# Performance work log

Measured on AMD Instinct MI355X. Metric: run time of the kernel, lower is better.

The kernel has to match this reference:

```python
import jax, jax.numpy as jnp
import numpy as np

N_NODES = 50000
N_EDGES = 800000
N_HIDDEN = 64
N_LAYER = 3
IN_DIM = 4


def setup_inputs() -> dict:
    key = jax.random.key(0)
    ks = jax.random.split(key, 10)
    x = jax.random.normal(ks[0], (N_NODES, IN_DIM), dtype=jnp.float32)
    edge_index = jax.random.randint(ks[1], (2, N_EDGES), 0, N_NODES, dtype=jnp.int64)
    # Glorot-style params matching pyg GCNConv (lin has no bias; conv adds bias after aggregation)
    def glorot(k, fan_in, fan_out):
        s = jnp.sqrt(6.0 / (fan_in + fan_out))
        return jax.random.uniform(k, (fan_in, fan_out), jnp.float32, -s, s)
    W_in = glorot(ks[2], IN_DIM, N_HIDDEN)
    b_in = jnp.zeros((N_HIDDEN,), jnp.float32)
    W_h = jnp.stack([glorot(jax.random.fold_in(ks[3], i), N_HIDDEN, N_HIDDEN) for i in range(N_LAYER)])
    b_h = jnp.zeros((N_LAYER, N_HIDDEN), jnp.float32)
    W_out = glorot(ks[4], N_HIDDEN, 1)
    b_out = jnp.zeros((1,), jnp.float32)
    return {"x": x, "edge_index": edge_index, "W_in": W_in, "b_in": b_in,
            "W_h": W_h, "b_h": b_h, "W_out": W_out, "b_out": b_out}


def _gcn_norm(edge_index, n_nodes):
    # add self-loops, compute symmetric norm D^{-1/2} (A+I) D^{-1/2}
    loop = jnp.arange(n_nodes, dtype=edge_index.dtype)
    src = jnp.concatenate([edge_index[0], loop])
    dst = jnp.concatenate([edge_index[1], loop])
    deg = jax.ops.segment_sum(jnp.ones_like(dst, dtype=jnp.float32), dst, num_segments=n_nodes)
    dinv = jax.lax.rsqrt(deg)  # deg >= 1 due to self-loops
    norm = dinv[src] * dinv[dst]
    return src, dst, norm


def _gcn_conv(x, W, b, src, dst, norm, n_nodes):
    h = x @ W                                   # [N, out]
    msg = h[src] * norm[:, None]                # gather + scale, [E+N, out]
    out = jax.ops.segment_sum(msg, dst, num_segments=n_nodes)  # scatter-add
    return out + b


def reference(x, edge_index, W_in, b_in, W_h, b_h, W_out, b_out):
    n = x.shape[0]
    src, dst, norm = _gcn_norm(edge_index, n)
    h = jax.nn.relu(_gcn_conv(x, W_in, b_in, src, dst, norm, n))
    for i in range(W_h.shape[0]):
        h = jax.nn.relu(_gcn_conv(h, W_h[i], b_h[i], src, dst, norm, n))
    return _gcn_conv(h, W_out, b_out, src, dst, norm, n)
```

## Files before the change

kernel.cpp:

```cpp
#include <hip/hip_runtime.h>
#include <hip/hip_bf16.h>


#define TPB 256
#define EPT 8
#define CHUNK (TPB * EPT)
typedef __hip_bfloat16 bf16;
#define B2F __bfloat162float

__global__ void k_zero_cnt(int* __restrict__ cnt, int n) {
    int i = blockIdx.x * blockDim.x + threadIdx.x;
    if (i < n) cnt[i] = 0;
}

__global__ void k_hist(const int* __restrict__ dst, int* __restrict__ cnt, int E, int n) {
    int e = blockIdx.x * blockDim.x + threadIdx.x;
    if (e < E) {
        int d = dst[e];
        if ((unsigned)d < (unsigned)n) atomicAdd(&cnt[d], 1);
    }
}

__global__ void k_blocksum(const int* __restrict__ cnt, int* __restrict__ bsum, int n) {
    __shared__ int s[TPB];
    int i = blockIdx.x * TPB + threadIdx.x;
    s[threadIdx.x] = (i < n) ? cnt[i] : 0;
    __syncthreads();
    for (int off = TPB / 2; off > 0; off >>= 1) {
        if (threadIdx.x < off) s[threadIdx.x] += s[threadIdx.x + off];
        __syncthreads();
    }
    if (threadIdx.x == 0) bsum[blockIdx.x] = s[0];
}

__global__ void k_scan_bsum(int* __restrict__ bsum, int nb) {
    __shared__ int s[TPB];
    int t = threadIdx.x;
    int v = (t < nb) ? bsum[t] : 0;
    s[t] = v;
    __syncthreads();
    for (int off = 1; off < TPB; off <<= 1) {
        int u = (t >= off) ? s[t - off] : 0;
        __syncthreads();
        s[t] += u;
        __syncthreads();
    }
    if (t < nb) bsum[t] = s[t] - v;
}

__global__ void k_scan_final(const int* __restrict__ cnt, const int* __restrict__ bsum,
                             int* __restrict__ row_start, int* __restrict__ cursor,
                             float* __restrict__ dinv, int n) {
    __shared__ int s[TPB];
    int t = threadIdx.x;
    int i = blockIdx.x * TPB + t;
    int v = (i < n) ? cnt[i] : 0;
    s[t] = v;
    __syncthreads();
    for (int off = 1; off < TPB; off <<= 1) {
        int u = (t >= off) ? s[t - off] : 0;
        __syncthreads();
        s[t] += u;
        __syncthreads();
    }
    if (i < n) {
        int excl = bsum[blockIdx.x] + s[t] - v;
        row_start[i] = excl;
        cursor[i] = excl;
        dinv[i] = rsqrtf((float)v + 1.0f);
        if (i == n - 1) row_start[n] = excl + v;
    }
}

__global__ void k_init_bcur(const int* __restrict__ row_start, int* __restrict__ bcur,
                            int B, int n) {
    int b = threadIdx.x;
    if (b < B) bcur[b] = row_start[min(b << 8, n)];
}

__global__ __launch_bounds__(TPB) void k_bin(
    const int* __restrict__ src, const int* __restrict__ dst,
    int* __restrict__ bcur, unsigned* __restrict__ staging, int E, int n) {
    __shared__ int hcnt[256];
    __shared__ int hbase[256];
    int tid = threadIdx.x;
    int e0 = blockIdx.x * CHUNK;
    hcnt[tid] = 0;
    __syncthreads();

    int eb[EPT];
    unsigned rec[EPT];
#pragma unroll
    for (int u = 0; u < EPT; ++u) {
        int e = e0 + u * TPB + tid;
        eb[u] = -1;
        if (e < E) {
            int d = dst[e], s = src[e];
            if ((unsigned)d < (unsigned)n && (unsigned)s < (unsigned)n) {
                eb[u] = d >> 8;
                rec[u] = (unsigned)s | ((unsigned)(d & 255) << 16);
                atomicAdd(&hcnt[eb[u]], 1);
            }
        }
    }
    __syncthreads();
    int c = hcnt[tid];
    hbase[tid] = (c > 0) ? atomicAdd(&bcur[tid], c) : 0;
    hcnt[tid] = 0;
    __syncthreads();
#pragma unroll
    for (int u = 0; u < EPT; ++u) {
        if (eb[u] >= 0) {
            int r = atomicAdd(&hcnt[eb[u]], 1);
            int pos = hbase[eb[u]] + r;
            if ((unsigned)pos < (unsigned)E) staging[pos] = rec[u];
        }
    }
}

__global__ __launch_bounds__(TPB) void k_unbin(
    const unsigned* __restrict__ staging, const int* __restrict__ row_start,
    int* __restrict__ cursor, unsigned short* __restrict__ bucket, int E, int n) {
    int b = blockIdx.x;
    int lo = row_start[min(b << 8, n)];
    int hi = row_start[min((b + 1) << 8, n)];
    lo = max(0, min(lo, E)); hi = max(lo, min(hi, E));
    for (int i = lo + threadIdx.x; i < hi; i += TPB) {
        unsigned r = staging[i];
        int d = min((b << 8) + (int)(r >> 16), n - 1);
        int pos = atomicAdd(&cursor[d], 1);
        if ((unsigned)pos < (unsigned)E) bucket[pos] = (unsigned short)(r & 0xffffu);
    }
}

__global__ void k_mm_in(const float* __restrict__ x, const float* __restrict__ W,
                        const float* __restrict__ dinv, bf16* __restrict__ g, int n) {
    int t = blockIdx.x * blockDim.x + threadIdx.x;
    if (t >= n * 64) return;
    int i = t >> 6, j = t & 63;
    float acc = 0.f;
#pragma unroll
    for (int k = 0; k < 4; ++k) acc = fmaf(x[i * 4 + k], W[k * 64 + j], acc);
    g[t] = __float2bfloat16(acc * dinv[i]);
}

__device__ __forceinline__ void acc_quad(float4& a, uint2 w) {
    a.x += __uint_as_float(w.x << 16);
    a.y += __uint_as_float(w.x & 0xffff0000u);
    a.z += __uint_as_float(w.y << 16);
    a.w += __uint_as_float(w.y & 0xffff0000u);
}

__device__ __forceinline__ void agg_row_quad(const bf16* __restrict__ g,
                                             const unsigned short* __restrict__ bucket,
                                             int k0, int k1, int d, float* __restrict__ sVp,
                                             int lane, unsigned nm1, unsigned Em1) {
    int grp = lane >> 4, i = lane & 15;
    float4 a = {0.f, 0.f, 0.f, 0.f};
    if (grp == 0) {
        uint2 w = *(const uint2*)(g + (size_t)d * 64 + 4 * i);
        acc_quad(a, w);
    }
    for (int base = k0; base < k1; base += 64) {
        int cnt = min(64, k1 - base);
        int rec = bucket[min((unsigned)(base + lane), Em1)];
        int k = 0;
        for (; k + 16 <= cnt; k += 16) {
            unsigned s0 = min((unsigned)__shfl(rec, k + 0 + grp), nm1);
            unsigned s1 = min((unsigned)__shfl(rec, k + 4 + grp), nm1);
            unsigned s2 = min((unsigned)__shfl(rec, k + 8 + grp), nm1);
            unsigned s3 = min((unsigned)__shfl(rec, k + 12 + grp), nm1);
            uint2 w0 = *(const uint2*)(g + (size_t)s0 * 64 + 4 * i);
            uint2 w1 = *(const uint2*)(g + (size_t)s1 * 64 + 4 * i);
            uint2 w2 = *(const uint2*)(g + (size_t)s2 * 64 + 4 * i);
            uint2 w3 = *(const uint2*)(g + (size_t)s3 * 64 + 4 * i);
            acc_quad(a, w0); acc_quad(a, w1); acc_quad(a, w2); acc_quad(a, w3);
        }
        for (; k < cnt; k += 4) {
            int e = k + grp;
            unsigned s = min((unsigned)__shfl(rec, min(e, 63)), nm1);
            uint2 w = *(const uint2*)(g + (size_t)s * 64 + 4 * i);
            if (e < cnt) acc_quad(a, w);
        }
    }
    ((float4*)(sVp + grp * 64))[i] = a;
}

__global__ __launch_bounds__(TPB) void k_gconv(
    const bf16* __restrict__ gIn, const float* __restrict__ dinv,
    const int* __restrict__ row_start, const unsigned short* __restrict__ bucket,
    const float* __restrict__ bias, const float* __restrict__ W,
    bf16* __restrict__ gOut, int n, int E) {
    __shared__ float sVp[4][4 * 64];
    int tid = threadIdx.x;
    int r = tid >> 6, j = tid & 63;
    int d = blockIdx.x * 4 + r;
    if (d >= n) return;
    float dd = dinv[d];
    int k0 = row_start[d], k1 = row_start[d + 1];
    k1 = min(k1, E); k0 = max(min(k0, k1), 0);
    agg_row_quad(gIn, bucket, k0, k1, d, sVp[r], j, (unsigned)(n - 1), (unsigned)(E - 1));
    float v = sVp[r][j] + sVp[r][64 + j] + sVp[r][128 + j] + sVp[r][192 + j];
    float a = fmaxf(fmaf(dd, v, bias[j]), 0.f);
    sVp[r][j] = a;
    const float4* ap = (const float4*)&sVp[r][0];
    float acc0 = 0.f, acc1 = 0.f, acc2 = 0.f, acc3 = 0.f;
#pragma unroll
    for (int k4 = 0; k4 < 16; ++k4) {
        float4 a4 = ap[k4];
        acc0 = fmaf(a4.x, W[(4 * k4 + 0) * 64 + j], acc0);
        acc1 = fmaf(a4.y, W[(4 * k4 + 1) * 64 + j], acc1);
        acc2 = fmaf(a4.z, W[(4 * k4 + 2) * 64 + j], acc2);
        acc3 = fmaf(a4.w, W[(4 * k4 + 3) * 64 + j], acc3);
    }
    float acc = (acc0 + acc1) + (acc2 + acc3);
    gOut[(size_t)d * 64 + j] = __float2bfloat16(acc * dd);
}

__global__ __launch_bounds__(TPB) void k_gconv_z(
    const bf16* __restrict__ gIn, const float* __restrict__ dinv,
    const int* __restrict__ row_start, const unsigned short* __restrict__ bucket,
    const float* __restrict__ bias, const float* __restrict__ Wout,
    float* __restrict__ zg, int n, int E) {
    __shared__ float sVp[4][4 * 64];
    int tid = threadIdx.x;
    int r = tid >> 6, j = tid & 63;
    int d = blockIdx.x * 4 + r;
    if (d >= n) return;
    float dd = dinv[d];
    int k0 = row_start[d], k1 = row_start[d + 1];
    k1 = min(k1, E); k0 = max(min(k0, k1), 0);
    agg_row_quad(gIn, bucket, k0, k1, d, sVp[r], j, (unsigned)(n - 1), (unsigned)(E - 1));
    float v = sVp[r][j] + sVp[r][64 + j] + sVp[r][128 + j] + sVp[r][192 + j];
    float a = fmaxf(fmaf(dd, v, bias[j]), 0.f) * Wout[j];
#pragma unroll
    for (int off = 32; off > 0; off >>= 1) a += __shfl_down(a, off);
    if (j == 0) zg[d] = a * dd;
}

__global__ __launch_bounds__(TPB) void k_out(
    const float* __restrict__ zg, const float* __restrict__ dinv,
    const int* __restrict__ row_start, const unsigned short* __restrict__ bucket,
    const float* __restrict__ b_out, float* __restrict__ out, int n, int E) {
    int t = blockIdx.x * blockDim.x + threadIdx.x;
    int d = t >> 6, lane = t & 63;
    if (d >= n) return;
    int k0 = row_start[d], k1 = row_start[d + 1];
    k1 = min(k1, E); k0 = max(min(k0, k1), 0);
    unsigned nm1 = (unsigned)(n - 1);
    float v = 0.f;
    for (int k = k0 + lane; k < k1; k += 64) {
        unsigned s = min((unsigned)bucket[k], nm1);
        v += zg[s];
    }
#pragma unroll
    for (int off = 32; off > 0; off >>= 1) v += __shfl_down(v, off);
    if (lane == 0) out[d] = fmaf(zg[d] + v, dinv[d], b_out[0]);
}

extern "C" void kernel_launch(void* const* d_in, const int* in_sizes, int n_in,
                              void* d_out, int out_size, void* d_ws, size_t ws_size,
                              hipStream_t stream) {
    const float* x     = (const float*)d_in[0];
    const int*   ei    = (const int*)d_in[1];
    const float* W_in  = (const float*)d_in[2];
    const float* b_in  = (const float*)d_in[3];
    const float* W_h   = (const float*)d_in[4];
    const float* b_h   = (const float*)d_in[5];
    const float* W_out = (const float*)d_in[6];
    const float* b_out = (const float*)d_in[7];
    float* out = (float*)d_out;

    int N = in_sizes[0] / 4;
    int E = in_sizes[1] / 2;
    const int* src = ei;
    const int* dst = ei + E;

    char* ws = (char*)d_ws;
    bf16* gA               = (bf16*)ws;           ws += (size_t)N * 64 * 2;
    bf16* gB               = (bf16*)ws;           ws += (size_t)N * 64 * 2;
    unsigned short* bucket = (unsigned short*)ws; ws += (size_t)E * 2;
    unsigned* staging      = (unsigned*)ws;       ws += (size_t)E * 4;
    int*  row_start        = (int*)ws;            ws += (size_t)(N + 1) * 4;
    int*  cursor           = (int*)ws;            ws += (size_t)N * 4;
    int*  cnt              = (int*)ws;            ws += (size_t)N * 4;
    float* dinv            = (float*)ws;          ws += (size_t)N * 4;
    float* zg              = (float*)ws;          ws += (size_t)N * 4;
    int*  bsum             = (int*)ws;            ws += 257 * 4;
    int*  bcur             = (int*)ws;

    int B   = (N + 255) >> 8;
    int gN  = (N + TPB - 1) / TPB;
    int gE  = (E + TPB - 1) / TPB;
    int gNF = (N * 64 + TPB - 1) / TPB;
    int gN4 = (N + 3) / 4;
    int gBin = (E + CHUNK - 1) / CHUNK;

    k_zero_cnt<<<gN, TPB, 0, stream>>>(cnt, N);
    k_hist<<<gE, TPB, 0, stream>>>(dst, cnt, E, N);
    k_blocksum<<<gN, TPB, 0, stream>>>(cnt, bsum, N);
    k_scan_bsum<<<1, TPB, 0, stream>>>(bsum, gN);
    k_scan_final<<<gN, TPB, 0, stream>>>(cnt, bsum, row_start, cursor, dinv, N);
    k_init_bcur<<<1, TPB, 0, stream>>>(row_start, bcur, B, N);
    k_bin<<<gBin, TPB, 0, stream>>>(src, dst, bcur, staging, E, N);
    k_unbin<<<B, TPB, 0, stream>>>(staging, row_start, cursor, bucket, E, N);

    k_mm_in<<<gNF, TPB, 0, stream>>>(x, W_in, dinv, gA, N);
    k_gconv<<<gN4, TPB, 0, stream>>>(gA, dinv, row_start, bucket, b_in, W_h, gB, N, E);
    k_gconv<<<gN4, TPB, 0, stream>>>(gB, dinv, row_start, bucket, b_h, W_h + 4096, gA, N, E);
    k_gconv<<<gN4, TPB, 0, stream>>>(gA, dinv, row_start, bucket, b_h + 64, W_h + 8192, gB, N, E);
    k_gconv_z<<<gN4, TPB, 0, stream>>>(gB, dinv, row_start, bucket, b_h + 128, W_out, zg, N, E);
    k_out<<<gN4, TPB, 0, stream>>>(zg, dinv, row_start, bucket, b_out, out, N, E);
}
```

Measured before the change: 310.4 us.

## Replace per-node histogram and global scan with bucket-level counting and in-block CSR build

Drops the per-node global histogram, the three-pass prefix scan and the bcur init. It now counts edges per 256-node bucket using shared-memory atomics and scans only 256 bucket totals. Each unbin block builds its own per-node counts, row offsets and dinv in shared memory, and places edges with shared-memory cursors instead of global atomics. This cuts kernel launches and global atomic traffic during graph preprocessing, but the staging array is now read twice in unbin and the approach only supports up to 256 buckets.

```diff
diff --git a/kernel.cpp b/kernel.cpp
--- a/kernel.cpp
+++ b/kernel.cpp
@@ -8,74 +8,46 @@
 typedef __hip_bfloat16 bf16;
 #define B2F __bfloat162float
 
-__global__ void k_zero_cnt(int* __restrict__ cnt, int n) {
-    int i = blockIdx.x * blockDim.x + threadIdx.x;
-    if (i < n) cnt[i] = 0;
-}
-
-__global__ void k_hist(const int* __restrict__ dst, int* __restrict__ cnt, int E, int n) {
-    int e = blockIdx.x * blockDim.x + threadIdx.x;
-    if (e < E) {
-        int d = dst[e];
-        if ((unsigned)d < (unsigned)n) atomicAdd(&cnt[d], 1);
-    }
-}
-
-__global__ void k_blocksum(const int* __restrict__ cnt, int* __restrict__ bsum, int n) {
-    __shared__ int s[TPB];
-    int i = blockIdx.x * TPB + threadIdx.x;
-    s[threadIdx.x] = (i < n) ? cnt[i] : 0;
-    __syncthreads();
-    for (int off = TPB / 2; off > 0; off >>= 1) {
-        if (threadIdx.x < off) s[threadIdx.x] += s[threadIdx.x + off];
-        __syncthreads();
-    }
-    if (threadIdx.x == 0) bsum[blockIdx.x] = s[0];
-}
-
-__global__ void k_scan_bsum(int* __restrict__ bsum, int nb) {
-    __shared__ int s[TPB];
+__global__ void k_zero_b(int* __restrict__ bktcnt) {
+    bktcnt[threadIdx.x] = 0;
+}
+
+__global__ __launch_bounds__(TPB) void k_bktcnt(
+    const int* __restrict__ dst, int* __restrict__ bktcnt, int E, int n) {
+    __shared__ int h[256];
+    int tid = threadIdx.x;
+    h[tid] = 0;
+    __syncthreads();
+    int e0 = blockIdx.x * CHUNK;
+#pragma unroll
+    for (int u = 0; u < EPT; ++u) {
+        int e = e0 + u * TPB + tid;
+        if (e < E) {
+            int d = dst[e];
+            if ((unsigned)d < (unsigned)n) atomicAdd(&h[d >> 8], 1);
+        }
+    }
+    __syncthreads();
+    if (h[tid]) atomicAdd(&bktcnt[tid], h[tid]);
+}
+
+__global__ void k_bktscan(const int* __restrict__ bktcnt, int* __restrict__ bktbase,
+                          int* __restrict__ bcur) {
+    __shared__ int s[256];
     int t = threadIdx.x;
-    int v = (t < nb) ? bsum[t] : 0;
+    int v = bktcnt[t];
     s[t] = v;
     __syncthreads();
-    for (int off = 1; off < TPB; off <<= 1) {
+    for (int off = 1; off < 256; off <<= 1) {
         int u = (t >= off) ? s[t - off] : 0;
         __syncthreads();
         s[t] += u;
         __syncthreads();
     }
-    if (t < nb) bsum[t] = s[t] - v;
-}
-
-__global__ void k_scan_final(const int* __restrict__ cnt, const int* __restrict__ bsum,
-                             int* __restrict__ row_start, int* __restrict__ cursor,
-                             float* __restrict__ dinv, int n) {
-    __shared__ int s[TPB];
-    int t = threadIdx.x;
-    int i = blockIdx.x * TPB + t;
-    int v = (i < n) ? cnt[i] : 0;
-    s[t] = v;
-    __syncthreads();
-    for (int off = 1; off < TPB; off <<= 1) {
-        int u = (t >= off) ? s[t - off] : 0;
-        __syncthreads();
-        s[t] += u;
-        __syncthreads();
-    }
-    if (i < n) {
-        int excl = bsum[blockIdx.x] + s[t] - v;
-        row_start[i] = excl;
-        cursor[i] = excl;
-        dinv[i] = rsqrtf((float)v + 1.0f);
-        if (i == n - 1) row_start[n] = excl + v;
-    }
-}
-
-__global__ void k_init_bcur(const int* __restrict__ row_start, int* __restrict__ bcur,
-                            int B, int n) {
-    int b = threadIdx.x;
-    if (b < B) bcur[b] = row_start[min(b << 8, n)];
+    int excl = s[t] - v;
+    bktbase[t] = excl;
+    bcur[t] = excl;
+    if (t == 255) bktbase[256] = s[t];
 }
 
 __global__ __launch_bounds__(TPB) void k_bin(
@@ -118,17 +90,47 @@
     }
 }
 
-__global__ __launch_bounds__(TPB) void k_unbin(
-    const unsigned* __restrict__ staging, const int* __restrict__ row_start,
-    int* __restrict__ cursor, unsigned short* __restrict__ bucket, int E, int n) {
-    int b = blockIdx.x;
-    int lo = row_start[min(b << 8, n)];
-    int hi = row_start[min((b + 1) << 8, n)];
+__global__ __launch_bounds__(TPB) void k_unbin2(
+    const unsigned* __restrict__ staging, const int* __restrict__ bktbase,
+    int* __restrict__ row_start, float* __restrict__ dinv,
+    unsigned short* __restrict__ bucket, int E, int n) {
+    __shared__ int cnt[256];
+    __shared__ int scn[256];
+    __shared__ int cur[256];
+    int b = blockIdx.x, tid = threadIdx.x;
+    int lo = bktbase[b], hi = bktbase[b + 1];
     lo = max(0, min(lo, E)); hi = max(lo, min(hi, E));
-    for (int i = lo + threadIdx.x; i < hi; i += TPB) {
+
+    cnt[tid] = 0;
+    __syncthreads();
+    for (int i = lo + tid; i < hi; i += TPB)
+        atomicAdd(&cnt[(staging[i] >> 16) & 255], 1);
+    __syncthreads();
+
+    int v = cnt[tid];
+    scn[tid] = v;
+    __syncthreads();
+    for (int off = 1; off < 256; off <<= 1) {
+        int u = (tid >= off) ? scn[tid - off] : 0;
+        __syncthreads();
+        scn[tid] += u;
+        __syncthreads();
+    }
+    int excl = scn[tid] - v;
+    int base = min(lo + excl, E);
+    cur[tid] = base;
+    int d = (b << 8) + tid;
+    if (d < n) {
+        row_start[d] = base;
+        dinv[d] = rsqrtf((float)v + 1.0f);
+        if (d == n - 1) row_start[n] = min(base + v, E);
+    }
+    __syncthreads();
+
+    for (int i = lo + tid; i < hi; i += TPB) {
         unsigned r = staging[i];
-        int d = min((b << 8) + (int)(r >> 16), n - 1);
-        int pos = atomicAdd(&cursor[d], 1);
+        int t = (r >> 16) & 255;
+        int pos = atomicAdd(&cur[t], 1);
         if ((unsigned)pos < (unsigned)E) bucket[pos] = (unsigned short)(r & 0xffffu);
     }
 }
@@ -282,28 +284,22 @@
     unsigned short* bucket = (unsigned short*)ws; ws += (size_t)E * 2;
     unsigned* staging      = (unsigned*)ws;       ws += (size_t)E * 4;
     int*  row_start        = (int*)ws;            ws += (size_t)(N + 1) * 4;
-    int*  cursor           = (int*)ws;            ws += (size_t)N * 4;
-    int*  cnt              = (int*)ws;            ws += (size_t)N * 4;
     float* dinv            = (float*)ws;          ws += (size_t)N * 4;
     float* zg              = (float*)ws;          ws += (size_t)N * 4;
-    int*  bsum             = (int*)ws;            ws += 257 * 4;
+    int*  bktcnt           = (int*)ws;            ws += 256 * 4;
+    int*  bktbase          = (int*)ws;            ws += 257 * 4;
     int*  bcur             = (int*)ws;
 
     int B   = (N + 255) >> 8;
-    int gN  = (N + TPB - 1) / TPB;
-    int gE  = (E + TPB - 1) / TPB;
     int gNF = (N * 64 + TPB - 1) / TPB;
     int gN4 = (N + 3) / 4;
     int gBin = (E + CHUNK - 1) / CHUNK;
 
-    k_zero_cnt<<<gN, TPB, 0, stream>>>(cnt, N);
-    k_hist<<<gE, TPB, 0, stream>>>(dst, cnt, E, N);
-    k_blocksum<<<gN, TPB, 0, stream>>>(cnt, bsum, N);
-    k_scan_bsum<<<1, TPB, 0, stream>>>(bsum, gN);
-    k_scan_final<<<gN, TPB, 0, stream>>>(cnt, bsum, row_start, cursor, dinv, N);
-    k_init_bcur<<<1, TPB, 0, stream>>>(row_start, bcur, B, N);
+    k_zero_b<<<1, 256, 0, stream>>>(bktcnt);
+    k_bktcnt<<<gBin, TPB, 0, stream>>>(dst, bktcnt, E, N);
+    k_bktscan<<<1, 256, 0, stream>>>(bktcnt, bktbase, bcur);
     k_bin<<<gBin, TPB, 0, stream>>>(src, dst, bcur, staging, E, N);
-    k_unbin<<<B, TPB, 0, stream>>>(staging, row_start, cursor, bucket, E, N);
+    k_unbin2<<<B, TPB, 0, stream>>>(staging, bktbase, row_start, dinv, bucket, E, N);
 
     k_mm_in<<<gNF, TPB, 0, stream>>>(x, W_in, dinv, gA, N);
     k_gconv<<<gN4, TPB, 0, stream>>>(gA, dinv, row_start, bucket, b_in, W_h, gB, N, E);
```

Result: faster. 273.5 us (-11.9%).
